# Kernel tuning notes

Measured on AMD Instinct MI355X. Metric: run time of the kernel, lower is better.

The kernel has to match this reference:

```python
import jax, jax.numpy as jnp
import numpy as np


def rotary_pos_emb(x):
    # x: [..., seq, dim], dim even. Interleaved (GPT-NeoX-style pairwise) rotary.
    dim, seq = x.shape[-1], x.shape[-2]
    ts = jnp.arange(0, dim, 2, dtype=jnp.float32)
    inv_freqs = 10000.0 ** (-ts / dim)
    grid = jnp.arange(seq, dtype=jnp.float32)[:, None] * inv_freqs[None, :]  # [s, dim//2]
    sin = jnp.repeat(jnp.sin(grid), 2, axis=-1).astype(x.dtype)  # [s, dim]
    cos = jnp.repeat(jnp.cos(grid), 2, axis=-1).astype(x.dtype)  # [s, dim]
    x1, x2 = x[..., ::2], x[..., 1::2]
    xs = jnp.stack([-x2, x1], axis=-1).reshape(x.shape)  # interleave (-x2, x1)
    return x * cos + xs * sin


def setup_inputs() -> dict:
    key = jax.random.key(0)
    kx, kq, kk, kv, ko = jax.random.split(key, 5)
    B, S, D = 2, 2048, 1024
    scale = 1.0 / np.sqrt(D)
    x = jax.random.normal(kx, (B, S, D), dtype=jnp.float32)
    mask = jnp.tril(jnp.ones((S, S), dtype=bool))  # causal
    Wq = jax.random.normal(kq, (D, D), dtype=jnp.float32) * scale
    Wk = jax.random.normal(kk, (D, D), dtype=jnp.float32) * scale
    Wv = jax.random.normal(kv, (D, D), dtype=jnp.float32) * scale
    Wo = jax.random.normal(ko, (D, D), dtype=jnp.float32) * scale
    return {"x": x, "mask": mask, "Wq": Wq, "Wk": Wk, "Wv": Wv, "Wo": Wo}


def reference(x, mask, Wq, Wk, Wv, Wo):
    H = 16
    POS_PORTION = 0.5
    B, S, D = x.shape
    K = D // H
    p = int(K * POS_PORTION)

    q = (x @ Wq) / (K ** 0.5)
    q = q.reshape(B, S, H, K).transpose(0, 2, 1, 3)  # b h l k
    q = jnp.concatenate([rotary_pos_emb(q[..., :p]), q[..., p:]], axis=-1)

    k = (x @ Wk).reshape(B, S, H, K).transpose(0, 2, 1, 3)
    k = jnp.concatenate([rotary_pos_emb(k[..., :p]), k[..., p:]], axis=-1)

    v = (x @ Wv).reshape(B, S, H, K).transpose(0, 2, 1, 3)

    logits = jnp.einsum('bhik,bhjk->bhij', q, k)
    # full-precision masked softmax
    l32 = logits.astype(jnp.float32)
    l32 = jnp.where(mask, l32, -1e30)
    a = jax.nn.softmax(l32, axis=-1).astype(logits.dtype)

    y = jnp.einsum('bhij,bhjv->bhiv', a, v)
    y = y.transpose(0, 2, 1, 3).reshape(B, S, D)  # b l (h v)
    return y @ Wo
```

## Files before the change

kernel.cpp:

```cpp
#include <hip/hip_runtime.h>
#include <cstdint>
#include <cstddef>

typedef __bf16 bf16;
typedef __bf16 bf16x8 __attribute__((ext_vector_type(8)));
typedef float  f32x4  __attribute__((ext_vector_type(4)));

#define B_  2
#define S_  2048
#define D_  1024
#define H_  16
#define KH  64

__device__ __forceinline__ void gload_lds16(const bf16* gp, bf16* lds_base) {
    __builtin_amdgcn_global_load_lds(
        (const __attribute__((address_space(1))) unsigned int*)gp,
        (__attribute__((address_space(3))) unsigned int*)lds_base,
        16, 0, 0);
}

__global__ __launch_bounds__(256) void prep(
    const float* __restrict__ x, bf16* __restrict__ xb,
    const float* __restrict__ Wq, const float* __restrict__ Wk,
    const float* __restrict__ Wv, const float* __restrict__ Wo,
    bf16* __restrict__ WqkvT, bf16* __restrict__ WoT)
{
    __shared__ bf16 tl[64][72];
    int z = blockIdx.x;
    if (z < 4096) {
        const int i = (z * 256 + threadIdx.x) * 4;
        const float4 v = *(const float4*)(x + i);
        union { int2 w; bf16 e[4]; } u;
        u.e[0] = (bf16)v.x; u.e[1] = (bf16)v.y;
        u.e[2] = (bf16)v.z; u.e[3] = (bf16)v.w;
        *(int2*)(xb + i) = u.w;
        return;
    }
    z -= 4096;
    const int zx = z & 15, zy = (z >> 4) & 15, zw = z >> 8;
    const float* src = (zw == 0) ? Wq : (zw == 1) ? Wk : (zw == 2) ? Wv : Wo;
    bf16* dst = (zw < 3) ? (WqkvT + (size_t)zw * D_ * D_) : WoT;
    const int r0 = zy * 64;
    const int c0 = zx * 64;
    const int t  = threadIdx.x;
    {
        const int r = t >> 2, cs = (t & 3) * 16;
        const float4* p = (const float4*)(src + (size_t)(r0 + r) * D_ + c0 + cs);
        float4 a0 = p[0], a1 = p[1], a2 = p[2], a3 = p[3];
        tl[cs +  0][r] = (bf16)a0.x; tl[cs +  1][r] = (bf16)a0.y;
        tl[cs +  2][r] = (bf16)a0.z; tl[cs +  3][r] = (bf16)a0.w;
        tl[cs +  4][r] = (bf16)a1.x; tl[cs +  5][r] = (bf16)a1.y;
        tl[cs +  6][r] = (bf16)a1.z; tl[cs +  7][r] = (bf16)a1.w;
        tl[cs +  8][r] = (bf16)a2.x; tl[cs +  9][r] = (bf16)a2.y;
        tl[cs + 10][r] = (bf16)a2.z; tl[cs + 11][r] = (bf16)a2.w;
        tl[cs + 12][r] = (bf16)a3.x; tl[cs + 13][r] = (bf16)a3.y;
        tl[cs + 14][r] = (bf16)a3.z; tl[cs + 15][r] = (bf16)a3.w;
    }
    __syncthreads();
    {
        const int c = t >> 2, rs = (t & 3) * 16;
        union { int4 v[2]; bf16 e[16]; } u;
#pragma unroll
        for (int i = 0; i < 16; ++i) u.e[i] = tl[c][rs + i];
        int4* p = (int4*)(dst + (size_t)(c0 + c) * D_ + r0 + rs);
        p[0] = u.v[0]; p[1] = u.v[1];
    }
}

template <int EPI, int BN>
__global__ __launch_bounds__(256, 2) void gemm_bt(
    const bf16* __restrict__ A, const bf16* __restrict__ BT,
    float* __restrict__ C, int N, int Kd,
    bf16* __restrict__ qp, bf16* __restrict__ kp, bf16* __restrict__ vp)
{
    constexpr int NJF = BN / 32;
    __shared__ bf16 As[128 * 64];
    __shared__ bf16 Bs[BN * 64];
    const int tid  = threadIdx.x;
    const int lane = tid & 63;
    const int wave = tid >> 6;
    const int l15  = lane & 15;
    const int quad = lane >> 4;
    const int m0 = blockIdx.y * 128;
    const int n0 = blockIdx.x * BN;
    const int wm = (wave >> 1) * 64;
    const int wn = (wave & 1) * (BN / 2);

    f32x4 acc[4][NJF];
#pragma unroll
    for (int i = 0; i < 4; ++i)
#pragma unroll
        for (int j = 0; j < NJF; ++j) acc[i][j] = f32x4{0.f, 0.f, 0.f, 0.f};

    for (int k0 = 0; k0 < Kd; k0 += 64) {
        __syncthreads();
#pragma unroll
        for (int c = 0; c < 4; ++c) {
            const int base  = wave * 4096 + c * 1024;
            const int flatb = base + lane * 16;
            const int row   = flatb >> 7;
            const int col   = (flatb & 127) >> 1;
            gload_lds16(A + (size_t)(m0 + row) * Kd + k0 + col, As + (base >> 1));
        }
#pragma unroll
        for (int c = 0; c < NJF; ++c) {
            const int base  = wave * (BN * 32) + c * 1024;
            const int flatb = base + lane * 16;
            const int row   = flatb >> 7;
            const int col   = (flatb & 127) >> 1;
            gload_lds16(BT + (size_t)(n0 + row) * Kd + k0 + col, Bs + (base >> 1));
        }
        __syncthreads();
#pragma unroll
        for (int kk = 0; kk < 64; kk += 32) {
            bf16x8 af[4], bfv[NJF];
#pragma unroll
            for (int i = 0; i < 4; ++i)
                af[i] = *(const bf16x8*)&As[(wm + i * 16 + l15) * 64 + kk + quad * 8];
#pragma unroll
            for (int j = 0; j < NJF; ++j)
                bfv[j] = *(const bf16x8*)&Bs[(wn + j * 16 + l15) * 64 + kk + quad * 8];
#pragma unroll
            for (int i = 0; i < 4; ++i)
#pragma unroll
                for (int j = 0; j < NJF; ++j)
                    acc[i][j] = __builtin_amdgcn_mfma_f32_16x16x32_bf16(
                        af[i], bfv[j], acc[i][j], 0, 0, 0);
        }
    }

#pragma unroll
    for (int i = 0; i < 4; ++i)
#pragma unroll
        for (int j = 0; j < NJF; ++j) {
            const int Rb = m0 + wm + i * 16 + quad * 4;
            const int Cc = n0 + wn + j * 16 + l15;
            if (EPI == 0) {
#pragma unroll
                for (int r = 0; r < 4; ++r)
                    C[(size_t)(Rb + r) * N + Cc] = acc[i][j][r];
            } else {
                const int sec = Cc >> 10, cc = Cc & 1023;
                const int h = cc >> 6, kd = cc & 63;
#pragma unroll
                for (int r = 0; r < 4; ++r) {
                    const int row = Rb + r;
                    const int b = row >> 11, s = row & (S_ - 1);
                    float v = acc[i][j][r];
                    if (sec == 0) v *= 0.125f;
                    if (sec <= 1 && j < 2) {
                        const float partner = __shfl_xor(v, 1);
                        const float inv = __builtin_exp2f(
                            -(float)(kd >> 1) * (13.28771237954945f / 16.f));
                        const float ang = (float)s * inv;
                        float sn, cn;
                        __sincosf(ang, &sn, &cn);
                        v = (l15 & 1) ? fmaf(partner, sn, v * cn)
                                      : fmaf(-partner, sn, v * cn);
                    }
                    if (sec == 2)
                        vp[((size_t)(b * H_ + h) * KH + kd) * S_ + s] = (bf16)v;
                    else if (sec == 1)
                        kp[((size_t)(b * H_ + h) * S_ + s) * KH + kd] = (bf16)v;
                    else
                        qp[((size_t)(b * H_ + h) * S_ + s) * KH + kd] = (bf16)v;
                }
            }
        }
}

__global__ __launch_bounds__(256, 2) void attn(
    const bf16* __restrict__ q, const bf16* __restrict__ k,
    const bf16* __restrict__ vt, bf16* __restrict__ y)
{
    __shared__ bf16 Ks[2][64 * 64];
    __shared__ bf16 VTs[2][64 * 64];
    __shared__ bf16 Ps[4][2][16][68];

    const int qtb = gridDim.x - 1 - blockIdx.x;
    const int bh  = blockIdx.y;
    const int b   = bh >> 4, h = bh & 15;
    const int t    = threadIdx.x;
    const int lane = t & 63, wave = t >> 6;
    const int l15  = lane & 15, quad = lane >> 4;
    const int qbase = qtb * 128;
    const int wrow  = qbase + wave * 32;

    const bf16* kbh = k  + (size_t)bh * S_ * KH;
    const bf16* vbh = vt + (size_t)bh * KH * S_;

    bf16x8 qf[2][2];
#pragma unroll
    for (int mi = 0; mi < 2; ++mi) {
        const bf16* qp = q + ((size_t)bh * S_ + wrow + mi * 16 + l15) * KH + quad * 8;
        qf[mi][0] = *(const bf16x8*)qp;
        qf[mi][1] = *(const bf16x8*)(qp + 32);
    }

    f32x4 accO[2][4];
    float lsum[2][4];
#pragma unroll
    for (int mi = 0; mi < 2; ++mi) {
#pragma unroll
        for (int j = 0; j < 4; ++j) accO[mi][j] = f32x4{0.f, 0.f, 0.f, 0.f};
#pragma unroll
        for (int r = 0; r < 4; ++r) lsum[mi][r] = 0.f;
    }

    const int srow = lane >> 3;
    const int sg   = (lane & 7) ^ srow;

    auto stage = [&](int jt, int bb) {
        const int j0 = jt * 64;
#pragma unroll
        for (int i = 0; i < 2; ++i) {
            const int c = wave * 2 + i;
            gload_lds16(kbh + (size_t)(j0 + c * 8 + srow) * KH + sg * 8,
                        &Ks[bb][c * 8 * 64]);
            gload_lds16(vbh + (size_t)(c * 8 + srow) * S_ + j0 + sg * 8,
                        &VTs[bb][c * 8 * 64]);
        }
    };

    const int nj = 2 * qtb + 2;
    stage(0, 0);
    for (int jt = 0; jt < nj; ++jt) {
        const int bb = jt & 1;
        const int j0 = jt * 64;
        __syncthreads();
        if (jt + 1 < nj) stage(jt + 1, bb ^ 1);

        f32x4 accS[2][4];
#pragma unroll
        for (int mi = 0; mi < 2; ++mi)
#pragma unroll
            for (int nb = 0; nb < 4; ++nb) accS[mi][nb] = f32x4{0.f, 0.f, 0.f, 0.f};
#pragma unroll
        for (int c = 0; c < 2; ++c) {
            bf16x8 kf[4];
#pragma unroll
            for (int nb = 0; nb < 4; ++nb)
                kf[nb] = *(const bf16x8*)
                    &Ks[bb][(nb * 16 + l15) * 64 + (((c * 4 + quad) ^ (l15 & 7)) * 8)];
#pragma unroll
            for (int mi = 0; mi < 2; ++mi)
#pragma unroll
                for (int nb = 0; nb < 4; ++nb)
                    accS[mi][nb] = __builtin_amdgcn_mfma_f32_16x16x32_bf16(
                        qf[mi][c], kf[nb], accS[mi][nb], 0, 0, 0);
        }

        if (j0 + 63 > wrow) {
#pragma unroll
            for (int mi = 0; mi < 2; ++mi)
#pragma unroll
                for (int nb = 0; nb < 4; ++nb)
#pragma unroll
                    for (int r = 0; r < 4; ++r) {
                        const int qi = wrow + mi * 16 + quad * 4 + r;
                        const int ki = j0 + nb * 16 + l15;
                        if (ki > qi) accS[mi][nb][r] = -1e30f;
                    }
        }

#pragma unroll
        for (int mi = 0; mi < 2; ++mi)
#pragma unroll
            for (int nb = 0; nb < 4; ++nb)
#pragma unroll
                for (int r = 0; r < 4; ++r) {
                    const float p = __expf(accS[mi][nb][r]);
                    lsum[mi][r] += p;
                    Ps[wave][mi][quad * 4 + r][nb * 16 + l15] = (bf16)p;
                }

#pragma unroll
        for (int c = 0; c < 2; ++c) {
            bf16x8 vf[4];
#pragma unroll
            for (int vb = 0; vb < 4; ++vb)
                vf[vb] = *(const bf16x8*)
                    &VTs[bb][(vb * 16 + l15) * 64 + (((c * 4 + quad) ^ (l15 & 7)) * 8)];
            bf16x8 pf[2];
#pragma unroll
            for (int mi = 0; mi < 2; ++mi)
                pf[mi] = *(const bf16x8*)&Ps[wave][mi][l15][c * 32 + quad * 8];
#pragma unroll
            for (int mi = 0; mi < 2; ++mi)
#pragma unroll
                for (int vb = 0; vb < 4; ++vb)
                    accO[mi][vb] = __builtin_amdgcn_mfma_f32_16x16x32_bf16(
                        pf[mi], vf[vb], accO[mi][vb], 0, 0, 0);
        }
    }

#pragma unroll
    for (int mi = 0; mi < 2; ++mi)
#pragma unroll
        for (int r = 0; r < 4; ++r) {
            float s = lsum[mi][r];
            s += __shfl_xor(s, 1);
            s += __shfl_xor(s, 2);
            s += __shfl_xor(s, 4);
            s += __shfl_xor(s, 8);
            lsum[mi][r] = s;
        }

#pragma unroll
    for (int mi = 0; mi < 2; ++mi)
#pragma unroll
        for (int vb = 0; vb < 4; ++vb)
#pragma unroll
            for (int r = 0; r < 4; ++r) {
                const int row = wrow + mi * 16 + quad * 4 + r;
                const int col = h * KH + vb * 16 + l15;
                y[((size_t)b * S_ + row) * D_ + col] = (bf16)(accO[mi][vb][r] / lsum[mi][r]);
            }
}

extern "C" void kernel_launch(void* const* d_in, const int* in_sizes, int n_in,
                              void* d_out, int out_size, void* d_ws, size_t ws_size,
                              hipStream_t stream)
{
    (void)in_sizes; (void)n_in; (void)out_size; (void)ws_size;
    const float* x  = (const float*)d_in[0];
    const float* Wq = (const float*)d_in[2];
    const float* Wk = (const float*)d_in[3];
    const float* Wv = (const float*)d_in[4];
    const float* Wo = (const float*)d_in[5];
    float* out = (float*)d_out;

    char* ws = (char*)d_ws;
    bf16* WqkvT = (bf16*)(ws + 0);
    bf16* WoT   = (bf16*)(ws + 6291456);
    bf16* xb    = (bf16*)(ws + 8388608);
    bf16* qw    = (bf16*)(ws + 16777216);
    bf16* kw    = (bf16*)(ws + 25165824);
    bf16* vtw   = (bf16*)(ws + 33554432);
    bf16* yw    = (bf16*)(ws + 41943040);

    hipLaunchKernelGGL(prep, dim3(5120), dim3(256), 0, stream,
                       x, xb, Wq, Wk, Wv, Wo, WqkvT, WoT);
    hipLaunchKernelGGL((gemm_bt<1, 128>), dim3(24, 32), dim3(256), 0, stream,
                       xb, WqkvT, (float*)nullptr, 3072, 1024, qw, kw, vtw);
    hipLaunchKernelGGL(attn, dim3(16, 32), dim3(256), 0, stream, qw, kw, vtw, yw);
    hipLaunchKernelGGL((gemm_bt<0, 64>), dim3(16, 32), dim3(256), 0, stream,
                       yw, WoT, out, 1024, 1024,
                       (bf16*)nullptr, (bf16*)nullptr, (bf16*)nullptr);
}
```

Measured before the change: 219.9 us.

## Pair causal query tiles per block, split RoPE into its own kernel

The attention kernel now handles two 64-row query tiles per block, pairing tile 31-p with tile p. This gives every block the same number of causal KV tiles, and the grid becomes a flat 512 blocks with a launch bound allowing 3 blocks per CU. Rotary embedding moves out of the QKV GEMM epilogue into a separate rope_qk kernel that rewrites the first 32 dims of q and k in place. The q scale now folds in log2(e), so softmax can use the hardware exp2 directly. The trade-off is an extra kernel launch plus an extra read and write of q and k, and the smaller per-wave tiles reuse each staged K/V tile less.

Result: faster. 211.7 us (-3.7%).

```diff
diff --git a/kernel.cpp b/kernel.cpp
--- a/kernel.cpp
+++ b/kernel.cpp
@@ -146,66 +146,63 @@
                 for (int r = 0; r < 4; ++r) {
                     const int row = Rb + r;
                     const int b = row >> 11, s = row & (S_ - 1);
-                    float v = acc[i][j][r];
-                    if (sec == 0) v *= 0.125f;
-                    if (sec <= 1 && j < 2) {
-                        const float partner = __shfl_xor(v, 1);
-                        const float inv = __builtin_exp2f(
-                            -(float)(kd >> 1) * (13.28771237954945f / 16.f));
-                        const float ang = (float)s * inv;
-                        float sn, cn;
-                        __sincosf(ang, &sn, &cn);
-                        v = (l15 & 1) ? fmaf(partner, sn, v * cn)
-                                      : fmaf(-partner, sn, v * cn);
-                    }
-                    if (sec == 2)
-                        vp[((size_t)(b * H_ + h) * KH + kd) * S_ + s] = (bf16)v;
+                    const float v = acc[i][j][r];
+                    if (sec == 0)
+                        qp[((size_t)(b * H_ + h) * S_ + s) * KH + kd] =
+                            (bf16)(v * 0.1803368801111204f);
                     else if (sec == 1)
                         kp[((size_t)(b * H_ + h) * S_ + s) * KH + kd] = (bf16)v;
                     else
-                        qp[((size_t)(b * H_ + h) * S_ + s) * KH + kd] = (bf16)v;
+                        vp[((size_t)(b * H_ + h) * KH + kd) * S_ + s] = (bf16)v;
                 }
             }
         }
 }
 
-__global__ __launch_bounds__(256, 2) void attn(
+__global__ __launch_bounds__(256) void rope_qk(bf16* __restrict__ q, bf16* __restrict__ k)
+{
+    const int tid   = blockIdx.x * blockDim.x + threadIdx.x;
+    const int which = tid >> 16;
+    const int rem   = tid & 65535;
+    const int s     = rem & (S_ - 1);
+    bf16* p = (which ? k : q) + (size_t)rem * KH;
+    union { int4 v[4]; bf16 e[32]; } u;
+    int4* pv = (int4*)p;
+#pragma unroll
+    for (int i = 0; i < 4; ++i) u.v[i] = pv[i];
+    const float l2_10000 = 13.28771237954945f;
+#pragma unroll
+    for (int i = 0; i < 16; ++i) {
+        const float inv = exp2f(-(float)i * (l2_10000 / 16.f));
+        const float ang = (float)s * inv;
+        const float sb = sinf(ang);
+        const float cb = cosf(ang);
+        const float x0 = (float)u.e[2 * i], x1 = (float)u.e[2 * i + 1];
+        u.e[2 * i]     = (bf16)(x0 * cb - x1 * sb);
+        u.e[2 * i + 1] = (bf16)(x1 * cb + x0 * sb);
+    }
+#pragma unroll
+    for (int i = 0; i < 4; ++i) pv[i] = u.v[i];
+}
+
+__global__ __launch_bounds__(256, 3) void attn(
     const bf16* __restrict__ q, const bf16* __restrict__ k,
     const bf16* __restrict__ vt, bf16* __restrict__ y)
 {
     __shared__ bf16 Ks[2][64 * 64];
     __shared__ bf16 VTs[2][64 * 64];
-    __shared__ bf16 Ps[4][2][16][68];
-
-    const int qtb = gridDim.x - 1 - blockIdx.x;
-    const int bh  = blockIdx.y;
-    const int b   = bh >> 4, h = bh & 15;
+    __shared__ bf16 Ps[4][16][68];
+
+    const int z  = blockIdx.x;
+    const int bh = z >> 4;
+    const int pp = z & 15;
+    const int b  = bh >> 4, h = bh & 15;
     const int t    = threadIdx.x;
     const int lane = t & 63, wave = t >> 6;
     const int l15  = lane & 15, quad = lane >> 4;
-    const int qbase = qtb * 128;
-    const int wrow  = qbase + wave * 32;
 
     const bf16* kbh = k  + (size_t)bh * S_ * KH;
     const bf16* vbh = vt + (size_t)bh * KH * S_;
-
-    bf16x8 qf[2][2];
-#pragma unroll
-    for (int mi = 0; mi < 2; ++mi) {
-        const bf16* qp = q + ((size_t)bh * S_ + wrow + mi * 16 + l15) * KH + quad * 8;
-        qf[mi][0] = *(const bf16x8*)qp;
-        qf[mi][1] = *(const bf16x8*)(qp + 32);
-    }
-
-    f32x4 accO[2][4];
-    float lsum[2][4];
-#pragma unroll
-    for (int mi = 0; mi < 2; ++mi) {
-#pragma unroll
-        for (int j = 0; j < 4; ++j) accO[mi][j] = f32x4{0.f, 0.f, 0.f, 0.f};
-#pragma unroll
-        for (int r = 0; r < 4; ++r) lsum[mi][r] = 0.f;
-    }
 
     const int srow = lane >> 3;
     const int sg   = (lane & 7) ^ srow;
@@ -222,100 +219,104 @@
         }
     };
 
-    const int nj = 2 * qtb + 2;
-    stage(0, 0);
-    for (int jt = 0; jt < nj; ++jt) {
-        const int bb = jt & 1;
-        const int j0 = jt * 64;
+#pragma unroll
+    for (int phase = 0; phase < 2; ++phase) {
+        const int qt   = phase ? pp : (31 - pp);
+        const int wrow = qt * 64 + wave * 16;
+        const int nj   = qt + 1;
+
+        bf16x8 qf[2];
+        {
+            const bf16* qp = q + ((size_t)bh * S_ + wrow + l15) * KH + quad * 8;
+            qf[0] = *(const bf16x8*)qp;
+            qf[1] = *(const bf16x8*)(qp + 32);
+        }
+
+        f32x4 accO[4];
+        float lsum[4];
+#pragma unroll
+        for (int j = 0; j < 4; ++j) accO[j] = f32x4{0.f, 0.f, 0.f, 0.f};
+#pragma unroll
+        for (int r = 0; r < 4; ++r) lsum[r] = 0.f;
+
         __syncthreads();
-        if (jt + 1 < nj) stage(jt + 1, bb ^ 1);
-
-        f32x4 accS[2][4];
-#pragma unroll
-        for (int mi = 0; mi < 2; ++mi)
-#pragma unroll
-            for (int nb = 0; nb < 4; ++nb) accS[mi][nb] = f32x4{0.f, 0.f, 0.f, 0.f};
-#pragma unroll
-        for (int c = 0; c < 2; ++c) {
-            bf16x8 kf[4];
+        stage(0, 0);
+        for (int jt = 0; jt < nj; ++jt) {
+            const int bb = jt & 1;
+            __syncthreads();
+            if (jt + 1 < nj) stage(jt + 1, bb ^ 1);
+
+            f32x4 accS[4];
+#pragma unroll
+            for (int nb = 0; nb < 4; ++nb) accS[nb] = f32x4{0.f, 0.f, 0.f, 0.f};
+#pragma unroll
+            for (int c = 0; c < 2; ++c) {
+                bf16x8 kf[4];
+#pragma unroll
+                for (int nb = 0; nb < 4; ++nb)
+                    kf[nb] = *(const bf16x8*)
+                        &Ks[bb][(nb * 16 + l15) * 64 + (((c * 4 + quad) ^ (l15 & 7)) * 8)];
+#pragma unroll
+                for (int nb = 0; nb < 4; ++nb)
+                    accS[nb] = __builtin_amdgcn_mfma_f32_16x16x32_bf16(
+                        qf[c], kf[nb], accS[nb], 0, 0, 0);
+            }
+
+            if (jt == nj - 1) {
+                const int j0 = jt * 64;
+#pragma unroll
+                for (int nb = 0; nb < 4; ++nb)
+#pragma unroll
+                    for (int r = 0; r < 4; ++r) {
+                        const int qi = wrow + quad * 4 + r;
+                        const int ki = j0 + nb * 16 + l15;
+                        if (ki > qi) accS[nb][r] = -1e30f;
+                    }
+            }
+
 #pragma unroll
             for (int nb = 0; nb < 4; ++nb)
-                kf[nb] = *(const bf16x8*)
-                    &Ks[bb][(nb * 16 + l15) * 64 + (((c * 4 + quad) ^ (l15 & 7)) * 8)];
-#pragma unroll
-            for (int mi = 0; mi < 2; ++mi)
-#pragma unroll
-                for (int nb = 0; nb < 4; ++nb)
-                    accS[mi][nb] = __builtin_amdgcn_mfma_f32_16x16x32_bf16(
-                        qf[mi][c], kf[nb], accS[mi][nb], 0, 0, 0);
-        }
-
-        if (j0 + 63 > wrow) {
-#pragma unroll
-            for (int mi = 0; mi < 2; ++mi)
-#pragma unroll
-                for (int nb = 0; nb < 4; ++nb)
-#pragma unroll
-                    for (int r = 0; r < 4; ++r) {
-                        const int qi = wrow + mi * 16 + quad * 4 + r;
-                        const int ki = j0 + nb * 16 + l15;
-                        if (ki > qi) accS[mi][nb][r] = -1e30f;
-                    }
-        }
-
-#pragma unroll
-        for (int mi = 0; mi < 2; ++mi)
-#pragma unroll
-            for (int nb = 0; nb < 4; ++nb)
 #pragma unroll
                 for (int r = 0; r < 4; ++r) {
-                    const float p = __expf(accS[mi][nb][r]);
-                    lsum[mi][r] += p;
-                    Ps[wave][mi][quad * 4 + r][nb * 16 + l15] = (bf16)p;
+                    const float p = __builtin_amdgcn_exp2f(accS[nb][r]);
+                    lsum[r] += p;
+                    Ps[wave][quad * 4 + r][nb * 16 + l15] = (bf16)p;
                 }
 
 #pragma unroll
-        for (int c = 0; c < 2; ++c) {
-            bf16x8 vf[4];
-#pragma unroll
-            for (int vb = 0; vb < 4; ++vb)
-                vf[vb] = *(const bf16x8*)
-                    &VTs[bb][(vb * 16 + l15) * 64 + (((c * 4 + quad) ^ (l15 & 7)) * 8)];
-            bf16x8 pf[2];
-#pragma unroll
-            for (int mi = 0; mi < 2; ++mi)
-                pf[mi] = *(const bf16x8*)&Ps[wave][mi][l15][c * 32 + quad * 8];
-#pragma unroll
-            for (int mi = 0; mi < 2; ++mi)
+            for (int c = 0; c < 2; ++c) {
+                bf16x8 vf[4];
 #pragma unroll
                 for (int vb = 0; vb < 4; ++vb)
-                    accO[mi][vb] = __builtin_amdgcn_mfma_f32_16x16x32_bf16(
-                        pf[mi], vf[vb], accO[mi][vb], 0, 0, 0);
-        }
-    }
-
-#pragma unroll
-    for (int mi = 0; mi < 2; ++mi)
+                    vf[vb] = *(const bf16x8*)
+                        &VTs[bb][(vb * 16 + l15) * 64 + (((c * 4 + quad) ^ (l15 & 7)) * 8)];
+                bf16x8 pf = *(const bf16x8*)&Ps[wave][l15][c * 32 + quad * 8];
+#pragma unroll
+                for (int vb = 0; vb < 4; ++vb)
+                    accO[vb] = __builtin_amdgcn_mfma_f32_16x16x32_bf16(
+                        pf, vf[vb], accO[vb], 0, 0, 0);
+            }
+        }
+
 #pragma unroll
         for (int r = 0; r < 4; ++r) {
-            float s = lsum[mi][r];
+            float s = lsum[r];
             s += __shfl_xor(s, 1);
             s += __shfl_xor(s, 2);
             s += __shfl_xor(s, 4);
             s += __shfl_xor(s, 8);
-            lsum[mi][r] = s;
-        }
-
-#pragma unroll
-    for (int mi = 0; mi < 2; ++mi)
+            lsum[r] = s;
+        }
+
 #pragma unroll
         for (int vb = 0; vb < 4; ++vb)
 #pragma unroll
             for (int r = 0; r < 4; ++r) {
-                const int row = wrow + mi * 16 + quad * 4 + r;
+                const int row = wrow + quad * 4 + r;
                 const int col = h * KH + vb * 16 + l15;
-                y[((size_t)b * S_ + row) * D_ + col] = (bf16)(accO[mi][vb][r] / lsum[mi][r]);
-            }
+                y[((size_t)b * S_ + row) * D_ + col] = (bf16)(accO[vb][r] / lsum[r]);
+            }
+    }
 }
 
 extern "C" void kernel_launch(void* const* d_in, const int* in_sizes, int n_in,
@@ -343,7 +344,8 @@
                        x, xb, Wq, Wk, Wv, Wo, WqkvT, WoT);
     hipLaunchKernelGGL((gemm_bt<1, 128>), dim3(24, 32), dim3(256), 0, stream,
                        xb, WqkvT, (float*)nullptr, 3072, 1024, qw, kw, vtw);
-    hipLaunchKernelGGL(attn, dim3(16, 32), dim3(256), 0, stream, qw, kw, vtw, yw);
+    hipLaunchKernelGGL(rope_qk, dim3(512), dim3(256), 0, stream, qw, kw);
+    hipLaunchKernelGGL(attn, dim3(512), dim3(256), 0, stream, qw, kw, vtw, yw);
     hipLaunchKernelGGL((gemm_bt<0, 64>), dim3(16, 32), dim3(256), 0, stream,
                        yw, WoT, out, 1024, 1024,
                        (bf16*)nullptr, (bf16*)nullptr, (bf16*)nullptr);
```

## Split attention into 64-row query tiles with balanced scheduling and MFMA row sums

Applied to the files above, without the earlier changes.

Attention blocks shrink from 256 to 128 threads and cover 64 query rows. A 1D grid pairs short and long causal tiles so per-CU work is more even. Q rotary moves from the GEMM epilogue into the attention prologue. The softmax scale is folded with log2(e) so the kernel can use a raw exp2. Row sums are computed by an extra MFMA against a ones vector, which replaces the shuffle reduction. The P buffer is XOR-swizzled to avoid LDS bank conflicts, at the cost of more K/V tile reloads per query row.

After: 203.3 us. 1.08x faster.

```diff
diff --git a/kernel.cpp b/kernel.cpp
--- a/kernel.cpp
+++ b/kernel.cpp
@@ -147,47 +147,67 @@
                     const int row = Rb + r;
                     const int b = row >> 11, s = row & (S_ - 1);
                     float v = acc[i][j][r];
-                    if (sec == 0) v *= 0.125f;
-                    if (sec <= 1 && j < 2) {
-                        const float partner = __shfl_xor(v, 1);
-                        const float inv = __builtin_exp2f(
-                            -(float)(kd >> 1) * (13.28771237954945f / 16.f));
-                        const float ang = (float)s * inv;
-                        float sn, cn;
-                        __sincosf(ang, &sn, &cn);
-                        v = (l15 & 1) ? fmaf(partner, sn, v * cn)
-                                      : fmaf(-partner, sn, v * cn);
+                    if (sec == 0) {
+                        qp[((size_t)(b * H_ + h) * S_ + s) * KH + kd] =
+                            (bf16)(v * 0.1803368801111204f);
+                    } else if (sec == 1) {
+                        if ((kd >> 4) < 2) {
+                            const float partner = __shfl_xor(v, 1);
+                            const float inv = __builtin_exp2f(
+                                -(float)(kd >> 1) * (13.28771237954945f / 16.f));
+                            const float ang = (float)s * inv;
+                            float sn, cn;
+                            __sincosf(ang, &sn, &cn);
+                            v = (l15 & 1) ? fmaf(partner, sn, v * cn)
+                                          : fmaf(-partner, sn, v * cn);
+                        }
+                        kp[((size_t)(b * H_ + h) * S_ + s) * KH + kd] = (bf16)v;
+                    } else {
+                        vp[((size_t)(b * H_ + h) * KH + kd) * S_ + s] = (bf16)v;
                     }
-                    if (sec == 2)
-                        vp[((size_t)(b * H_ + h) * KH + kd) * S_ + s] = (bf16)v;
-                    else if (sec == 1)
-                        kp[((size_t)(b * H_ + h) * S_ + s) * KH + kd] = (bf16)v;
-                    else
-                        qp[((size_t)(b * H_ + h) * S_ + s) * KH + kd] = (bf16)v;
                 }
             }
         }
 }
 
-__global__ __launch_bounds__(256, 2) void attn(
+__global__ __launch_bounds__(128, 2) void attn(
     const bf16* __restrict__ q, const bf16* __restrict__ k,
     const bf16* __restrict__ vt, bf16* __restrict__ y)
 {
     __shared__ bf16 Ks[2][64 * 64];
     __shared__ bf16 VTs[2][64 * 64];
-    __shared__ bf16 Ps[4][2][16][68];
-
-    const int qtb = gridDim.x - 1 - blockIdx.x;
-    const int bh  = blockIdx.y;
-    const int b   = bh >> 4, h = bh & 15;
+    __shared__ bf16 Ps[2][2][16][64];
+
+    const int z  = blockIdx.x;
+    const int v_ = z & 7;
+    const int u_ = (z >> 3) & 31;
+    const int w_ = z >> 8;
+    const int bh = u_;
+    const int qt = (w_ == 0) ? v_ : (w_ == 1) ? (15 - v_)
+                 : (w_ == 2) ? (16 + v_) : (31 - v_);
+    const int b  = bh >> 4, h = bh & 15;
     const int t    = threadIdx.x;
     const int lane = t & 63, wave = t >> 6;
     const int l15  = lane & 15, quad = lane >> 4;
-    const int qbase = qtb * 128;
-    const int wrow  = qbase + wave * 32;
+    const int wrow = qt * 64 + wave * 32;
 
     const bf16* kbh = k  + (size_t)bh * S_ * KH;
     const bf16* vbh = vt + (size_t)bh * KH * S_;
+
+    const int srow = lane >> 3;
+    const int sg   = (lane & 7) ^ srow;
+
+    auto stage = [&](int jt, int bb) {
+        const int j0 = jt * 64;
+#pragma unroll
+        for (int i = 0; i < 4; ++i) {
+            const int c = wave * 4 + i;
+            gload_lds16(kbh + (size_t)(j0 + c * 8 + srow) * KH + sg * 8,
+                        &Ks[bb][c * 8 * 64]);
+            gload_lds16(vbh + (size_t)(c * 8 + srow) * S_ + j0 + sg * 8,
+                        &VTs[bb][c * 8 * 64]);
+        }
+    };
 
     bf16x8 qf[2][2];
 #pragma unroll
@@ -195,38 +215,35 @@
         const bf16* qp = q + ((size_t)bh * S_ + wrow + mi * 16 + l15) * KH + quad * 8;
         qf[mi][0] = *(const bf16x8*)qp;
         qf[mi][1] = *(const bf16x8*)(qp + 32);
-    }
-
-    f32x4 accO[2][4];
-    float lsum[2][4];
+        const float s = (float)(wrow + mi * 16 + l15);
+#pragma unroll
+        for (int tt = 0; tt < 4; ++tt) {
+            const int i = quad * 4 + tt;
+            const float inv = exp2f(-(float)i * (13.28771237954945f / 16.f));
+            const float ang = s * inv;
+            const float sn = sinf(ang), cn = cosf(ang);
+            const float x0 = (float)qf[mi][0][2 * tt], x1 = (float)qf[mi][0][2 * tt + 1];
+            qf[mi][0][2 * tt]     = (bf16)(x0 * cn - x1 * sn);
+            qf[mi][0][2 * tt + 1] = (bf16)(x1 * cn + x0 * sn);
+        }
+    }
+
+    bf16x8 ones;
+#pragma unroll
+    for (int i = 0; i < 8; ++i) ones[i] = (bf16)1.0f;
+
+    f32x4 accO[2][4], lacc[2];
 #pragma unroll
     for (int mi = 0; mi < 2; ++mi) {
 #pragma unroll
         for (int j = 0; j < 4; ++j) accO[mi][j] = f32x4{0.f, 0.f, 0.f, 0.f};
-#pragma unroll
-        for (int r = 0; r < 4; ++r) lsum[mi][r] = 0.f;
-    }
-
-    const int srow = lane >> 3;
-    const int sg   = (lane & 7) ^ srow;
-
-    auto stage = [&](int jt, int bb) {
-        const int j0 = jt * 64;
-#pragma unroll
-        for (int i = 0; i < 2; ++i) {
-            const int c = wave * 2 + i;
-            gload_lds16(kbh + (size_t)(j0 + c * 8 + srow) * KH + sg * 8,
-                        &Ks[bb][c * 8 * 64]);
-            gload_lds16(vbh + (size_t)(c * 8 + srow) * S_ + j0 + sg * 8,
-                        &VTs[bb][c * 8 * 64]);
-        }
-    };
-
-    const int nj = 2 * qtb + 2;
+        lacc[mi] = f32x4{0.f, 0.f, 0.f, 0.f};
+    }
+
+    const int nj = qt + 1;
     stage(0, 0);
     for (int jt = 0; jt < nj; ++jt) {
         const int bb = jt & 1;
-        const int j0 = jt * 64;
         __syncthreads();
         if (jt + 1 < nj) stage(jt + 1, bb ^ 1);
 
@@ -250,7 +267,8 @@
                         qf[mi][c], kf[nb], accS[mi][nb], 0, 0, 0);
         }
 
-        if (j0 + 63 > wrow) {
+        if (jt == nj - 1) {
+            const int j0 = jt * 64;
 #pragma unroll
             for (int mi = 0; mi < 2; ++mi)
 #pragma unroll
@@ -269,9 +287,10 @@
             for (int nb = 0; nb < 4; ++nb)
 #pragma unroll
                 for (int r = 0; r < 4; ++r) {
-                    const float p = __expf(accS[mi][nb][r]);
-                    lsum[mi][r] += p;
-                    Ps[wave][mi][quad * 4 + r][nb * 16 + l15] = (bf16)p;
+                    const float p = __builtin_amdgcn_exp2f(accS[mi][nb][r]);
+                    const int row = quad * 4 + r;
+                    Ps[wave][mi][row][(((nb * 2 + (l15 >> 3)) ^ (row & 7)) * 8) + (l15 & 7)]
+                        = (bf16)p;
                 }
 
 #pragma unroll
@@ -284,38 +303,34 @@
             bf16x8 pf[2];
 #pragma unroll
             for (int mi = 0; mi < 2; ++mi)
-                pf[mi] = *(const bf16x8*)&Ps[wave][mi][l15][c * 32 + quad * 8];
-#pragma unroll
-            for (int mi = 0; mi < 2; ++mi)
+                pf[mi] = *(const bf16x8*)
+                    &Ps[wave][mi][l15][((c * 4 + quad) ^ (l15 & 7)) * 8];
+#pragma unroll
+            for (int mi = 0; mi < 2; ++mi) {
 #pragma unroll
                 for (int vb = 0; vb < 4; ++vb)
                     accO[mi][vb] = __builtin_amdgcn_mfma_f32_16x16x32_bf16(
                         pf[mi], vf[vb], accO[mi][vb], 0, 0, 0);
-        }
-    }
-
-#pragma unroll
-    for (int mi = 0; mi < 2; ++mi)
-#pragma unroll
-        for (int r = 0; r < 4; ++r) {
-            float s = lsum[mi][r];
-            s += __shfl_xor(s, 1);
-            s += __shfl_xor(s, 2);
-            s += __shfl_xor(s, 4);
-            s += __shfl_xor(s, 8);
-            lsum[mi][r] = s;
-        }
-
-#pragma unroll
-    for (int mi = 0; mi < 2; ++mi)
+                lacc[mi] = __builtin_amdgcn_mfma_f32_16x16x32_bf16(
+                    pf[mi], ones, lacc[mi], 0, 0, 0);
+            }
+        }
+    }
+
+#pragma unroll
+    for (int mi = 0; mi < 2; ++mi) {
+        float rinv[4];
+#pragma unroll
+        for (int r = 0; r < 4; ++r) rinv[r] = 1.0f / lacc[mi][r];
 #pragma unroll
         for (int vb = 0; vb < 4; ++vb)
 #pragma unroll
             for (int r = 0; r < 4; ++r) {
                 const int row = wrow + mi * 16 + quad * 4 + r;
                 const int col = h * KH + vb * 16 + l15;
-                y[((size_t)b * S_ + row) * D_ + col] = (bf16)(accO[mi][vb][r] / lsum[mi][r]);
+                y[((size_t)b * S_ + row) * D_ + col] = (bf16)(accO[mi][vb][r] * rinv[r]);
             }
+    }
 }
 
 extern "C" void kernel_launch(void* const* d_in, const int* in_sizes, int n_in,
@@ -343,7 +358,7 @@
                        x, xb, Wq, Wk, Wv, Wo, WqkvT, WoT);
     hipLaunchKernelGGL((gemm_bt<1, 128>), dim3(24, 32), dim3(256), 0, stream,
                        xb, WqkvT, (float*)nullptr, 3072, 1024, qw, kw, vtw);
-    hipLaunchKernelGGL(attn, dim3(16, 32), dim3(256), 0, stream, qw, kw, vtw, yw);
+    hipLaunchKernelGGL(attn, dim3(1024), dim3(128), 0, stream, qw, kw, vtw, yw);
     hipLaunchKernelGGL((gemm_bt<0, 64>), dim3(16, 32), dim3(256), 0, stream,
                        yw, WoT, out, 1024, 1024,
                        (bf16*)nullptr, (bf16*)nullptr, (bf16*)nullptr);
```
